# Performance work log

Measured on AMD Instinct MI355X. Metric: run time of the kernel, lower is better.

The kernel has to match this reference:

```python
import jax, jax.numpy as jnp
import numpy as np

DIM, E, K, H = 1024, 8, 2, 4096

def setup_inputs() -> dict:
    key = jax.random.key(0)
    ks = jax.random.split(key, 5)
    s_in = 1.0 / np.sqrt(DIM)
    s_h = 1.0 / np.sqrt(H)
    return {
        "x": jax.random.normal(ks[0], (4, 2048, DIM), dtype=jnp.float32),
        "Wr": jax.random.normal(ks[1], (DIM, E), dtype=jnp.float32) * s_in,
        "W1": jax.random.normal(ks[2], (E, DIM, H), dtype=jnp.float32) * s_in,
        "b1": jnp.zeros((E, H), dtype=jnp.float32),
        "W2": jax.random.normal(ks[3], (E, H, DIM), dtype=jnp.float32) * s_h,
        "b2": jnp.zeros((E, DIM), dtype=jnp.float32),
    }

def reference(x, Wr, W1, b1, W2, b2):
    batch, seq, dim = x.shape
    x_flat = x.reshape(-1, dim)                      # [T, D]
    logits = x_flat @ Wr                             # [T, E]
    w, ind = jax.lax.top_k(logits, K)                # [T, K]
    w = jax.nn.softmax(w, axis=-1)
    # combine[t, e] = sum_i w[t, i] * (ind[t, i] == e)
    combine = jnp.einsum('tke,tk->te', jax.nn.one_hot(ind, E, dtype=x.dtype), w)  # [T, E]

    def body(acc, params):
        W1e, b1e, W2e, b2e, ce = params
        h = jax.nn.gelu(x_flat @ W1e + b1e, approximate=False)  # exact GELU (torch nn.GELU default)
        y = h @ W2e + b2e                                        # [T, D]
        return acc + ce[:, None] * y, None

    out0 = jnp.zeros_like(x_flat)
    out, _ = jax.lax.scan(body, out0, (W1, b1, W2, b2, combine.T))
    return out.reshape(batch, seq, dim)
```

## Files before the change

kernel.cpp:

```cpp
#include <hip/hip_runtime.h>
#include <hip/hip_bf16.h>

#define TDIM 1024
#define NEXP 8
#define NHID 4096

typedef __hip_bfloat16 bf16;
typedef __attribute__((ext_vector_type(8))) short bf16x8;
typedef __attribute__((ext_vector_type(8))) unsigned short u16x8;
typedef __attribute__((ext_vector_type(4))) float f32x4;

__device__ __forceinline__ void gload_lds16(void* lds, const void* g) {
  __builtin_amdgcn_global_load_lds(
      (const __attribute__((address_space(1))) unsigned int*)g,
      (__attribute__((address_space(3))) unsigned int*)lds, 16, 0, 0);
}

__device__ __forceinline__ unsigned short f2bf_bits(float f) {
  __hip_bfloat16 b = __float2bfloat16(f);
  unsigned short u;
  __builtin_memcpy(&u, &b, 2);
  return u;
}

__device__ __forceinline__ float bf2f(unsigned short u) {
  union { unsigned int i; float f; } c;
  c.i = ((unsigned int)u) << 16;
  return c.f;
}

__device__ __forceinline__ void cvt_chunk(const float* __restrict__ src, bf16* __restrict__ dst,
                                          int c, int kqShift, int nMask, int rowLen) {
  const int kq = c >> kqShift;
  const int n = c & nMask;
  const float* s = src + ((size_t)kq * 8) * rowLen + n;
  u16x8 o;
#pragma unroll
  for (int j = 0; j < 8; ++j) o[j] = f2bf_bits(s[(size_t)j * rowLen]);
  *reinterpret_cast<u16x8*>(dst + (size_t)c * 8) = o;
}

__global__ __launch_bounds__(256) void prep_kernel(
    const float* __restrict__ W1, bf16* __restrict__ W1C, const float* __restrict__ x,
    bf16* __restrict__ xb, const float* __restrict__ Wr, int* __restrict__ idx,
    float* __restrict__ wtok, int* __restrict__ cnt, int T) {
  __shared__ float xs[4][1024];
  const int pb = blockIdx.x;
  const int tid = threadIdx.x;
  if (pb < 4096) {
    const int id = pb * 256 + tid;
#pragma unroll
    for (int v = 0; v < 4; ++v) cvt_chunk(W1, W1C, id + v * (1 << 20), 12, 4095, 4096);
  } else {
    const int p = pb - 4096;
    const int wave = p * 4 + (tid >> 6);
    const int lane = tid & 63;
    if (wave >= T) return;
    float* xrow = xs[tid >> 6];
    const float4* xr4 = reinterpret_cast<const float4*>(x + (size_t)wave * TDIM);
    bf16* xbrow = xb + (size_t)wave * TDIM;
#pragma unroll
    for (int i = 0; i < TDIM / 256; ++i) {
      float4 xv = xr4[lane + i * 64];
      ushort4 o;
      o.x = f2bf_bits(xv.x);
      o.y = f2bf_bits(xv.y);
      o.z = f2bf_bits(xv.z);
      o.w = f2bf_bits(xv.w);
      *reinterpret_cast<ushort4*>(xbrow + (lane + i * 64) * 4) = o;
      *reinterpret_cast<float4*>(&xrow[(lane + i * 64) * 4]) = xv;
    }
    float acc[NEXP];
#pragma unroll
    for (int e = 0; e < NEXP; ++e) acc[e] = 0.f;
    const float4* wr4 = reinterpret_cast<const float4*>(Wr);
#pragma unroll
    for (int i = 0; i < TDIM / 64; ++i) {
      float xv = xrow[lane + i * 64];
      float4 wa = wr4[(lane + i * 64) * 2];
      float4 wb = wr4[(lane + i * 64) * 2 + 1];
      acc[0] += xv * wa.x;
      acc[1] += xv * wa.y;
      acc[2] += xv * wa.z;
      acc[3] += xv * wa.w;
      acc[4] += xv * wb.x;
      acc[5] += xv * wb.y;
      acc[6] += xv * wb.z;
      acc[7] += xv * wb.w;
    }
#pragma unroll
    for (int e = 0; e < NEXP; ++e) {
      float v = acc[e];
#pragma unroll
      for (int s = 32; s; s >>= 1) v += __shfl_xor(v, s);
      acc[e] = v;
    }
    if (lane == 0) {
      int e0 = 0;
      float l0 = acc[0];
      for (int e = 1; e < NEXP; ++e)
        if (acc[e] > l0) { l0 = acc[e]; e0 = e; }
      int e1 = -1;
      float l1 = -INFINITY;
      for (int e = 0; e < NEXP; ++e)
        if (e != e0 && acc[e] > l1) { l1 = acc[e]; e1 = e; }
      float z = __expf(l1 - l0);
      idx[wave * 2] = e0;
      idx[wave * 2 + 1] = e1;
      wtok[wave * 2] = 1.f / (1.f + z);
      wtok[wave * 2 + 1] = z / (1.f + z);
      atomicAdd(&cnt[e0], 1);
      atomicAdd(&cnt[e1], 1);
    }
  }
}

__global__ void scan_kernel(const int* __restrict__ cnt, int* __restrict__ offs) {
  if (threadIdx.x == 0 && blockIdx.x == 0) {
    int s = 0;
    for (int e = 0; e < NEXP; ++e) { offs[e] = s; s += cnt[e]; }
  }
}

__global__ void build_perm_kernel(const int* __restrict__ idx, const int* __restrict__ offs,
                                  int* __restrict__ fill, int* __restrict__ perm,
                                  int* __restrict__ islot, int T) {
  int t = blockIdx.x * blockDim.x + threadIdx.x;
  if (t >= T) return;
#pragma unroll
  for (int k = 0; k < 2; ++k) {
    int e = idx[t * 2 + k];
    int p = offs[e] + atomicAdd(&fill[e], 1);
    perm[p] = t;
    islot[t * 2 + k] = p;
  }
}

template <int KD, int ND, bool GATHER, bool GELU, bool CONV>
__global__ __launch_bounds__(512, 2) void moe_gemm8(
    const bf16* __restrict__ A, const bf16* __restrict__ BC, const float* __restrict__ bias,
    const int* __restrict__ perm, const int* __restrict__ cnt, const int* __restrict__ offs,
    bf16* __restrict__ Dst, int nm, int nn, const float* __restrict__ Wsrc,
    bf16* __restrict__ Wdst) {
  __shared__ short lds[65536];

  const int nwg = NEXP * nm * nn;
  const int bid = blockIdx.x;
  if (CONV && bid >= nwg) {
    const int id = (bid - nwg) * 512 + threadIdx.x;
#pragma unroll
    for (int v = 0; v < 8; ++v) cvt_chunk(Wsrc, Wdst, id + v * (1 << 19), 10, 1023, 1024);
    return;
  }
  const int wg = (bid & 7) * (nwg >> 3) + (bid >> 3);
  const int e = wg / (nm * nn);
  const int rem = wg % (nm * nn);
  const int mb = rem / nn, nb = rem % nn;

  const int ce = cnt[e];
  const int m0 = mb * 256;
  if (m0 >= ce) return;
  const int base = offs[e];
  const int n0 = nb * 256;
  const int tid = threadIdx.x;
  const int lane = tid & 63;
  const int wid = tid >> 6;
  const int wm = wid >> 2, wn = wid & 3;
  const int lcol = lane & 15;
  const int lkg = (lane >> 4) * 8;

  const int kxs0 = ((lkg << 1) ^ ((lcol & 7) << 4)) >> 1;
  const int kxs1 = (((lkg + 32) << 1) ^ ((lcol & 7) << 4)) >> 1;
  int aRow[4], bRow[2];
#pragma unroll
  for (int mm = 0; mm < 4; ++mm) aRow[mm] = (wm * 64 + mm * 16 + lcol) << 6;
#pragma unroll
  for (int n2 = 0; n2 < 2; ++n2) bRow[n2] = (wn * 32 + n2 * 16 + lcol) << 6;

  const bf16* aP[2][2];
  const bf16* bP[2][2];
#pragma unroll
  for (int h = 0; h < 2; ++h)
#pragma unroll
    for (int i = 0; i < 2; ++i) {
      int s = tid + i * 512;
      int srow = s >> 3;
      int ksrc = (s & 7) ^ (srow & 7);
      int grow = m0 + h * 128 + srow;
      if (grow > ce - 1) grow = ce - 1;
      size_t arow = GATHER ? (size_t)perm[base + grow] : (size_t)(base + grow);
      aP[h][i] = A + arow * KD + ksrc * 8;
      bP[h][i] = BC + (size_t)e * KD * ND + ((size_t)ksrc * ND + (n0 + h * 128 + srow)) * 8;
    }

  f32x4 acc[8][4];
#pragma unroll
  for (int m = 0; m < 8; ++m)
#pragma unroll
    for (int n = 0; n < 4; ++n) acc[m][n] = (f32x4){0.f, 0.f, 0.f, 0.f};

  bf16x8 fA[4][2], fB[2][2];

#define STAGE(SBUF, OP, HF, kA, kB)                                                  \
  {                                                                                  \
    char* sd = (char*)lds + (SBUF) * 65536 + (OP) * 32768 + (HF) * 16384 + tid * 16; \
    if (OP) {                                                                        \
      gload_lds16(sd, bP[HF][0] + (kB));                                             \
      gload_lds16(sd + 8192, bP[HF][1] + (kB));                                      \
    } else {                                                                         \
      gload_lds16(sd, aP[HF][0] + (kA));                                             \
      gload_lds16(sd + 8192, aP[HF][1] + (kA));                                      \
    }                                                                                \
  }

#define PHASE(QM, QN, RA, RB, SOP, SHF, SBUF, CBUF, kA, kB, DO_VM)                   \
  {                                                                                  \
    STAGE(SBUF, SOP, SHF, kA, kB);                                                   \
    if (DO_VM) asm volatile("s_waitcnt vmcnt(6)" ::: "memory");                      \
    __builtin_amdgcn_s_barrier();                                                    \
    asm volatile("" ::: "memory");                                                   \
    if (RA) {                                                                        \
      const short* Ab = lds + (CBUF) * 32768 + (QM) * 8192;                          \
      _Pragma("unroll") for (int mm = 0; mm < 4; ++mm) {                             \
        fA[mm][0] = *(const bf16x8*)(Ab + aRow[mm] + kxs0);                          \
        fA[mm][1] = *(const bf16x8*)(Ab + aRow[mm] + kxs1);                          \
      }                                                                              \
    }                                                                                \
    if (RB) {                                                                        \
      const short* Bb = lds + (CBUF) * 32768 + 16384 + (QN) * 8192;                  \
      _Pragma("unroll") for (int n2 = 0; n2 < 2; ++n2) {                             \
        fB[n2][0] = *(const bf16x8*)(Bb + bRow[n2] + kxs0);                          \
        fB[n2][1] = *(const bf16x8*)(Bb + bRow[n2] + kxs1);                          \
      }                                                                              \
    }                                                                                \
    asm volatile("s_waitcnt lgkmcnt(0)" ::: "memory");                               \
    __builtin_amdgcn_s_setprio(1);                                                   \
    _Pragma("unroll") for (int mm = 0; mm < 4; ++mm)                                 \
        _Pragma("unroll") for (int n2 = 0; n2 < 2; ++n2) {                           \
      acc[(QM) * 4 + mm][(QN) * 2 + n2] = __builtin_amdgcn_mfma_f32_16x16x32_bf16(   \
          fA[mm][0], fB[n2][0], acc[(QM) * 4 + mm][(QN) * 2 + n2], 0, 0, 0);         \
      acc[(QM) * 4 + mm][(QN) * 2 + n2] = __builtin_amdgcn_mfma_f32_16x16x32_bf16(   \
          fA[mm][1], fB[n2][1], acc[(QM) * 4 + mm][(QN) * 2 + n2], 0, 0, 0);         \
    }                                                                                \
    __builtin_amdgcn_s_setprio(0);                                                   \
  }

  STAGE(0, 0, 0, 0, 0);
  STAGE(0, 1, 0, 0, 0);
  STAGE(0, 0, 1, 0, 0);
  STAGE(0, 1, 1, 0, 0);

  const int NI = KD / 128;
  for (int itv = 0; itv < NI; ++itv) {
    const int k1 = itv * 128 + 64;
    int k2 = itv * 128 + 128;
    if (k2 >= KD) k2 = 0;
    const int k1B = k1 * ND, k2B = k2 * ND;
    PHASE(0, 0, 1, 1, 0, 0, 1, 0, k1, k1B, 1)
    PHASE(1, 0, 1, 0, 1, 0, 1, 0, k1, k1B, 1)
    PHASE(1, 1, 0, 1, 0, 1, 1, 0, k1, k1B, 1)
    PHASE(0, 1, 1, 0, 1, 1, 1, 0, k1, k1B, 0)
    PHASE(0, 0, 1, 1, 0, 0, 0, 1, k2, k2B, 1)
    PHASE(1, 0, 1, 0, 1, 0, 0, 1, k2, k2B, 1)
    PHASE(1, 1, 0, 1, 0, 1, 0, 1, k2, k2B, 1)
    PHASE(0, 1, 1, 0, 1, 1, 0, 1, k2, k2B, 0)
  }
#undef PHASE
#undef STAGE

  float bv[4];
#pragma unroll
  for (int ni = 0; ni < 4; ++ni)
    bv[ni] = bias[e * ND + n0 + (ni >> 1) * 128 + wn * 32 + (ni & 1) * 16 + lcol];
  const int lr4 = (lane >> 4) * 4;
#pragma unroll
  for (int mi = 0; mi < 8; ++mi) {
    const int rbase = m0 + (mi >> 2) * 128 + wm * 64 + (mi & 3) * 16 + lr4;
#pragma unroll
    for (int r = 0; r < 4; ++r) {
      int grow = rbase + r;
      if (grow < ce) {
        bf16* drow = Dst + (size_t)(base + grow) * ND;
#pragma unroll
        for (int ni = 0; ni < 4; ++ni) {
          int col = n0 + (ni >> 1) * 128 + wn * 32 + (ni & 1) * 16 + lcol;
          float v = acc[mi][ni][r] + bv[ni];
          if (GELU) v = 0.5f * v * (1.0f + erff(v * 0.70710678118654752f));
          drow[col] = __float2bfloat16(v);
        }
      }
    }
  }
}

__global__ void combine_kernel(const bf16* __restrict__ y, const int* __restrict__ islot,
                               const float* __restrict__ wtok, float* __restrict__ out) {
  const int t = blockIdx.x;
  const int d = threadIdx.x * 4;
  const int s0 = islot[t * 2], s1 = islot[t * 2 + 1];
  const float w0 = wtok[t * 2], w1 = wtok[t * 2 + 1];
  ushort4 ya = *reinterpret_cast<const ushort4*>(y + (size_t)s0 * TDIM + d);
  ushort4 yb = *reinterpret_cast<const ushort4*>(y + (size_t)s1 * TDIM + d);
  float4 o;
  o.x = w0 * bf2f(ya.x) + w1 * bf2f(yb.x);
  o.y = w0 * bf2f(ya.y) + w1 * bf2f(yb.y);
  o.z = w0 * bf2f(ya.z) + w1 * bf2f(yb.z);
  o.w = w0 * bf2f(ya.w) + w1 * bf2f(yb.w);
  *reinterpret_cast<float4*>(out + (size_t)t * TDIM + d) = o;
}

extern "C" void kernel_launch(void* const* d_in, const int* in_sizes, int n_in, void* d_out,
                              int out_size, void* d_ws, size_t ws_size, hipStream_t stream) {
  const float* x = (const float*)d_in[0];
  const float* Wr = (const float*)d_in[1];
  const float* W1 = (const float*)d_in[2];
  const float* b1 = (const float*)d_in[3];
  const float* W2 = (const float*)d_in[4];
  const float* b2 = (const float*)d_in[5];
  float* out = (float*)d_out;
  const int T = in_sizes[0] / TDIM;

  size_t off = 0;
  auto alloc = [&](size_t bytes) {
    void* q = (char*)d_ws + off;
    off += (bytes + 255) & ~(size_t)255;
    return q;
  };
  bf16* xb = (bf16*)alloc((size_t)T * TDIM * 2);
  bf16* W1C = (bf16*)alloc((size_t)NEXP * TDIM * NHID * 2);
  bf16* W2C = (bf16*)alloc((size_t)NEXP * TDIM * NHID * 2);
  bf16* h = (bf16*)alloc((size_t)2 * T * NHID * 2);
  int* idx = (int*)alloc((size_t)T * 2 * 4);
  float* wtok = (float*)alloc((size_t)T * 2 * 4);
  int* perm = (int*)alloc((size_t)T * 2 * 4);
  int* islot = (int*)alloc((size_t)T * 2 * 4);
  int* cnt = (int*)alloc(256);
  int* fill = cnt + 8;
  int* offs = cnt + 16;
  bf16* y = W1C;

  hipMemsetAsync(cnt, 0, 64, stream);

  prep_kernel<<<6144, 256, 0, stream>>>(W1, W1C, x, xb, Wr, idx, wtok, cnt, T);
  scan_kernel<<<1, 64, 0, stream>>>(cnt, offs);
  build_perm_kernel<<<(T + 255) / 256, 256, 0, stream>>>(idx, offs, fill, perm, islot, T);

  moe_gemm8<TDIM, NHID, true, true, true><<<NEXP * 32 * 16 + 1024, 512, 0, stream>>>(
      xb, W1C, b1, perm, cnt, offs, h, 32, 16, W2, W2C);
  moe_gemm8<NHID, TDIM, false, false, false><<<NEXP * 32 * 4, 512, 0, stream>>>(
      h, W2C, b2, perm, cnt, offs, y, 32, 4, nullptr, nullptr);

  combine_kernel<<<T, 256, 0, stream>>>(y, islot, wtok, out);
}
```

Measured before the change: 775.2 us.

## Replace 256x256 phased MoE GEMM with simpler 128x128 double-buffered tile kernel

Swaps the 512-thread, 256x256-tile MoE GEMM for a 256-thread, 128x128-tile kernel. The old kernel used an 8-phase LDS pipeline with swizzling. The new one uses a plain K=32 double-buffered loop with one barrier per step, and a selectable mb/nb-major block order. The aim is more workgroups, smaller LDS use and simpler scheduling, but each tile reuses less data and hits more barriers. The number of m-tiles per expert now caps expert capacity at 4096 rows.

```diff
diff --git a/kernel.cpp b/kernel.cpp
--- a/kernel.cpp
+++ b/kernel.cpp
@@ -136,18 +136,19 @@
   }
 }
 
-template <int KD, int ND, bool GATHER, bool GELU, bool CONV>
-__global__ __launch_bounds__(512, 2) void moe_gemm8(
+template <int KD, int ND, bool GATHER, bool GELU, bool CONV, bool MBMAJOR>
+__global__ __launch_bounds__(256) void moe_gemm97(
     const bf16* __restrict__ A, const bf16* __restrict__ BC, const float* __restrict__ bias,
     const int* __restrict__ perm, const int* __restrict__ cnt, const int* __restrict__ offs,
     bf16* __restrict__ Dst, int nm, int nn, const float* __restrict__ Wsrc,
     bf16* __restrict__ Wdst) {
-  __shared__ short lds[65536];
+  __shared__ short sA[2][4096];
+  __shared__ short sB[2][4096];
 
   const int nwg = NEXP * nm * nn;
   const int bid = blockIdx.x;
   if (CONV && bid >= nwg) {
-    const int id = (bid - nwg) * 512 + threadIdx.x;
+    const int id = (bid - nwg) * 256 + threadIdx.x;
 #pragma unroll
     for (int v = 0; v < 8; ++v) cvt_chunk(Wsrc, Wdst, id + v * (1 << 19), 10, 1023, 1024);
     return;
@@ -155,142 +156,94 @@
   const int wg = (bid & 7) * (nwg >> 3) + (bid >> 3);
   const int e = wg / (nm * nn);
   const int rem = wg % (nm * nn);
-  const int mb = rem / nn, nb = rem % nn;
+  const int mb = MBMAJOR ? rem / nn : rem % nm;
+  const int nb = MBMAJOR ? rem % nn : rem / nm;
 
   const int ce = cnt[e];
-  const int m0 = mb * 256;
+  const int m0 = mb * 128;
   if (m0 >= ce) return;
   const int base = offs[e];
-  const int n0 = nb * 256;
+  const int n0 = nb * 128;
   const int tid = threadIdx.x;
   const int lane = tid & 63;
   const int wid = tid >> 6;
-  const int wm = wid >> 2, wn = wid & 3;
+  const int wm = wid >> 1, wn = wid & 1;
   const int lcol = lane & 15;
-  const int lkg = (lane >> 4) * 8;
-
-  const int kxs0 = ((lkg << 1) ^ ((lcol & 7) << 4)) >> 1;
-  const int kxs1 = (((lkg + 32) << 1) ^ ((lcol & 7) << 4)) >> 1;
-  int aRow[4], bRow[2];
-#pragma unroll
-  for (int mm = 0; mm < 4; ++mm) aRow[mm] = (wm * 64 + mm * 16 + lcol) << 6;
-#pragma unroll
-  for (int n2 = 0; n2 < 2; ++n2) bRow[n2] = (wn * 32 + n2 * 16 + lcol) << 6;
-
-  const bf16* aP[2][2];
-  const bf16* bP[2][2];
-#pragma unroll
-  for (int h = 0; h < 2; ++h)
-#pragma unroll
-    for (int i = 0; i < 2; ++i) {
-      int s = tid + i * 512;
-      int srow = s >> 3;
-      int ksrc = (s & 7) ^ (srow & 7);
-      int grow = m0 + h * 128 + srow;
-      if (grow > ce - 1) grow = ce - 1;
-      size_t arow = GATHER ? (size_t)perm[base + grow] : (size_t)(base + grow);
-      aP[h][i] = A + arow * KD + ksrc * 8;
-      bP[h][i] = BC + (size_t)e * KD * ND + ((size_t)ksrc * ND + (n0 + h * 128 + srow)) * 8;
-    }
-
-  f32x4 acc[8][4];
-#pragma unroll
-  for (int m = 0; m < 8; ++m)
+  const int lk = lane >> 4;
+
+  const bf16* aP[2];
+  const bf16* bP[2];
+#pragma unroll
+  for (int i = 0; i < 2; ++i) {
+    int t = tid + i * 256;
+    int srow = t >> 2, ks = t & 3;
+    int grow = m0 + srow;
+    if (grow > ce - 1) grow = ce - 1;
+    size_t arow = GATHER ? (size_t)perm[base + grow] : (size_t)(base + grow);
+    aP[i] = A + arow * KD + ks * 8;
+    int jo = t >> 7, brow = t & 127;
+    bP[i] = BC + (size_t)e * KD * ND + ((size_t)jo * ND + (n0 + brow)) * 8;
+  }
+
+  f32x4 acc[4][4];
+#pragma unroll
+  for (int m = 0; m < 4; ++m)
 #pragma unroll
     for (int n = 0; n < 4; ++n) acc[m][n] = (f32x4){0.f, 0.f, 0.f, 0.f};
 
-  bf16x8 fA[4][2], fB[2][2];
-
-#define STAGE(SBUF, OP, HF, kA, kB)                                                  \
-  {                                                                                  \
-    char* sd = (char*)lds + (SBUF) * 65536 + (OP) * 32768 + (HF) * 16384 + tid * 16; \
-    if (OP) {                                                                        \
-      gload_lds16(sd, bP[HF][0] + (kB));                                             \
-      gload_lds16(sd + 8192, bP[HF][1] + (kB));                                      \
-    } else {                                                                         \
-      gload_lds16(sd, aP[HF][0] + (kA));                                             \
-      gload_lds16(sd + 8192, aP[HF][1] + (kA));                                      \
-    }                                                                                \
-  }
-
-#define PHASE(QM, QN, RA, RB, SOP, SHF, SBUF, CBUF, kA, kB, DO_VM)                   \
-  {                                                                                  \
-    STAGE(SBUF, SOP, SHF, kA, kB);                                                   \
-    if (DO_VM) asm volatile("s_waitcnt vmcnt(6)" ::: "memory");                      \
-    __builtin_amdgcn_s_barrier();                                                    \
-    asm volatile("" ::: "memory");                                                   \
-    if (RA) {                                                                        \
-      const short* Ab = lds + (CBUF) * 32768 + (QM) * 8192;                          \
-      _Pragma("unroll") for (int mm = 0; mm < 4; ++mm) {                             \
-        fA[mm][0] = *(const bf16x8*)(Ab + aRow[mm] + kxs0);                          \
-        fA[mm][1] = *(const bf16x8*)(Ab + aRow[mm] + kxs1);                          \
-      }                                                                              \
-    }                                                                                \
-    if (RB) {                                                                        \
-      const short* Bb = lds + (CBUF) * 32768 + 16384 + (QN) * 8192;                  \
-      _Pragma("unroll") for (int n2 = 0; n2 < 2; ++n2) {                             \
-        fB[n2][0] = *(const bf16x8*)(Bb + bRow[n2] + kxs0);                          \
-        fB[n2][1] = *(const bf16x8*)(Bb + bRow[n2] + kxs1);                          \
-      }                                                                              \
-    }                                                                                \
-    asm volatile("s_waitcnt lgkmcnt(0)" ::: "memory");                               \
-    __builtin_amdgcn_s_setprio(1);                                                   \
-    _Pragma("unroll") for (int mm = 0; mm < 4; ++mm)                                 \
-        _Pragma("unroll") for (int n2 = 0; n2 < 2; ++n2) {                           \
-      acc[(QM) * 4 + mm][(QN) * 2 + n2] = __builtin_amdgcn_mfma_f32_16x16x32_bf16(   \
-          fA[mm][0], fB[n2][0], acc[(QM) * 4 + mm][(QN) * 2 + n2], 0, 0, 0);         \
-      acc[(QM) * 4 + mm][(QN) * 2 + n2] = __builtin_amdgcn_mfma_f32_16x16x32_bf16(   \
-          fA[mm][1], fB[n2][1], acc[(QM) * 4 + mm][(QN) * 2 + n2], 0, 0, 0);         \
-    }                                                                                \
-    __builtin_amdgcn_s_setprio(0);                                                   \
-  }
-
-  STAGE(0, 0, 0, 0, 0);
-  STAGE(0, 1, 0, 0, 0);
-  STAGE(0, 0, 1, 0, 0);
-  STAGE(0, 1, 1, 0, 0);
-
-  const int NI = KD / 128;
-  for (int itv = 0; itv < NI; ++itv) {
-    const int k1 = itv * 128 + 64;
-    int k2 = itv * 128 + 128;
-    if (k2 >= KD) k2 = 0;
-    const int k1B = k1 * ND, k2B = k2 * ND;
-    PHASE(0, 0, 1, 1, 0, 0, 1, 0, k1, k1B, 1)
-    PHASE(1, 0, 1, 0, 1, 0, 1, 0, k1, k1B, 1)
-    PHASE(1, 1, 0, 1, 0, 1, 1, 0, k1, k1B, 1)
-    PHASE(0, 1, 1, 0, 1, 1, 1, 0, k1, k1B, 0)
-    PHASE(0, 0, 1, 1, 0, 0, 0, 1, k2, k2B, 1)
-    PHASE(1, 0, 1, 0, 1, 0, 0, 1, k2, k2B, 1)
-    PHASE(1, 1, 0, 1, 0, 1, 0, 1, k2, k2B, 1)
-    PHASE(0, 1, 1, 0, 1, 1, 0, 1, k2, k2B, 0)
-  }
-#undef PHASE
+#define STAGE(BUF, k0)                                                    \
+  {                                                                       \
+    gload_lds16((char*)sA[BUF] + tid * 16, aP[0] + (k0));                 \
+    gload_lds16((char*)sA[BUF] + 4096 + tid * 16, aP[1] + (k0));          \
+    gload_lds16((char*)sB[BUF] + tid * 16, bP[0] + (size_t)(k0)*ND);      \
+    gload_lds16((char*)sB[BUF] + 4096 + tid * 16, bP[1] + (size_t)(k0)*ND); \
+  }
+
+  STAGE(0, 0);
+  __syncthreads();
+
+  const int NT = KD / 32;
+  for (int kt = 0; kt < NT; ++kt) {
+    const int cur = kt & 1;
+    if (kt + 1 < NT) STAGE(cur ^ 1, (kt + 1) * 32);
+    const short* Ab = sA[cur];
+    const short* Bb = sB[cur];
+    bf16x8 fA[4], fB[4];
+#pragma unroll
+    for (int n = 0; n < 4; ++n)
+      fB[n] = *(const bf16x8*)(Bb + ((size_t)lk * 128 + wn * 64 + n * 16 + lcol) * 8);
+#pragma unroll
+    for (int m = 0; m < 4; ++m)
+      fA[m] = *(const bf16x8*)(Ab + ((size_t)(wm * 64 + m * 16 + lcol)) * 32 + lk * 8);
+#pragma unroll
+    for (int m = 0; m < 4; ++m)
+#pragma unroll
+      for (int n = 0; n < 4; ++n)
+        acc[m][n] = __builtin_amdgcn_mfma_f32_16x16x32_bf16(fA[m], fB[n], acc[m][n], 0, 0, 0);
+    __syncthreads();
+  }
 #undef STAGE
 
   float bv[4];
 #pragma unroll
-  for (int ni = 0; ni < 4; ++ni)
-    bv[ni] = bias[e * ND + n0 + (ni >> 1) * 128 + wn * 32 + (ni & 1) * 16 + lcol];
-  const int lr4 = (lane >> 4) * 4;
-#pragma unroll
-  for (int mi = 0; mi < 8; ++mi) {
-    const int rbase = m0 + (mi >> 2) * 128 + wm * 64 + (mi & 3) * 16 + lr4;
+  for (int n = 0; n < 4; ++n) bv[n] = bias[e * ND + n0 + wn * 64 + n * 16 + lcol];
+  const int lr4 = lk * 4;
+#pragma unroll
+  for (int m = 0; m < 4; ++m)
 #pragma unroll
     for (int r = 0; r < 4; ++r) {
-      int grow = rbase + r;
+      int grow = m0 + wm * 64 + m * 16 + lr4 + r;
       if (grow < ce) {
         bf16* drow = Dst + (size_t)(base + grow) * ND;
 #pragma unroll
-        for (int ni = 0; ni < 4; ++ni) {
-          int col = n0 + (ni >> 1) * 128 + wn * 32 + (ni & 1) * 16 + lcol;
-          float v = acc[mi][ni][r] + bv[ni];
+        for (int n = 0; n < 4; ++n) {
+          int col = n0 + wn * 64 + n * 16 + lcol;
+          float v = acc[m][n][r] + bv[n];
           if (GELU) v = 0.5f * v * (1.0f + erff(v * 0.70710678118654752f));
           drow[col] = __float2bfloat16(v);
         }
       }
     }
-  }
 }
 
 __global__ void combine_kernel(const bf16* __restrict__ y, const int* __restrict__ islot,
@@ -345,10 +298,10 @@
   scan_kernel<<<1, 64, 0, stream>>>(cnt, offs);
   build_perm_kernel<<<(T + 255) / 256, 256, 0, stream>>>(idx, offs, fill, perm, islot, T);
 
-  moe_gemm8<TDIM, NHID, true, true, true><<<NEXP * 32 * 16 + 1024, 512, 0, stream>>>(
-      xb, W1C, b1, perm, cnt, offs, h, 32, 16, W2, W2C);
-  moe_gemm8<NHID, TDIM, false, false, false><<<NEXP * 32 * 4, 512, 0, stream>>>(
-      h, W2C, b2, perm, cnt, offs, y, 32, 4, nullptr, nullptr);
+  moe_gemm97<TDIM, NHID, true, true, true, false><<<NEXP * 32 * 32 + 2048, 256, 0, stream>>>(
+      xb, W1C, b1, perm, cnt, offs, h, 32, 32, W2, W2C);
+  moe_gemm97<NHID, TDIM, false, false, false, true><<<NEXP * 32 * 8, 256, 0, stream>>>(
+      h, W2C, b2, perm, cnt, offs, y, 32, 8, nullptr, nullptr);
 
   combine_kernel<<<T, 256, 0, stream>>>(y, islot, wtok, out);
 }
```

New measurement: 876.2 us. 1.13x slower.
